# Performance work log

Hardware: AMD Instinct MI355X
Metric: run time of the kernel (lower is better)

## Reference

```python
import jax, jax.numpy as jnp
import numpy as np
from jax import lax

SCALE = 2
NUM_POINTS = 4

def conv2d(x, w, b, pad):
    # x: [B,C,H,W], w: [O,I,kh,kw]
    y = lax.conv_general_dilated(x, w, (1, 1), [(pad, pad), (pad, pad)],
                                 dimension_numbers=("NCHW", "OIHW", "NCHW"))
    return y + b[None, :, None, None]

def grid_sample_border(feat, grid):
    # feat: [B,C,H,W]; grid: [B,Hg,Wg,2] in [-1,1] (x,y), align_corners=False,
    # padding_mode='border' (coordinates clipped before interpolation, as in torch).
    B, C, H, W = feat.shape
    Hg, Wg = grid.shape[1], grid.shape[2]
    gx = jnp.clip((grid[..., 0] + 1.0) * W / 2.0 - 0.5, 0.0, W - 1.0)
    gy = jnp.clip((grid[..., 1] + 1.0) * H / 2.0 - 0.5, 0.0, H - 1.0)
    x0 = jnp.floor(gx); y0 = jnp.floor(gy)
    fx = (gx - x0).reshape(B, 1, -1)
    fy = (gy - y0).reshape(B, 1, -1)
    x0i = jnp.clip(x0.astype(jnp.int32), 0, W - 1)
    y0i = jnp.clip(y0.astype(jnp.int32), 0, H - 1)
    x1i = jnp.clip(x0i + 1, 0, W - 1)
    y1i = jnp.clip(y0i + 1, 0, H - 1)
    featf = feat.reshape(B, C, H * W)
    def gather(yi, xi):
        idx = (yi * W + xi).reshape(B, 1, -1)
        return jnp.take_along_axis(featf, idx, axis=2)  # [B,C,Hg*Wg]
    v00 = gather(y0i, x0i); v01 = gather(y0i, x1i)
    v10 = gather(y1i, x0i); v11 = gather(y1i, x1i)
    out = (v00 * (1 - fx) * (1 - fy) + v01 * fx * (1 - fy)
           + v10 * (1 - fx) * fy + v11 * fx * fy)
    return out.reshape(B, C, Hg, Wg)

def setup_inputs() -> dict:
    key = jax.random.key(0)
    ks = jax.random.split(key, 8)
    B, Cin, Cout, H, W = 8, 256, 256, 64, 64
    high_feat = jax.random.normal(ks[0], (B, Cin, H, W), jnp.float32)
    low_feat = jax.random.normal(ks[1], (B, Cout, H * SCALE, W * SCALE), jnp.float32)
    W1 = jax.random.normal(ks[2], (Cin, Cin + Cout, 1, 1), jnp.float32) * 0.02
    b1 = jnp.zeros((Cin,), jnp.float32)
    # original inits offset_conv2 to zeros; use small random to exercise deformable sampling
    W2 = jax.random.normal(ks[3], (NUM_POINTS * 2, Cin, 3, 3), jnp.float32) * 0.01
    b2 = jnp.zeros((NUM_POINTS * 2,), jnp.float32)
    Wf = jax.random.normal(ks[4], (Cout, Cin, 1, 1), jnp.float32) * 0.05
    bf = jnp.zeros((Cout,), jnp.float32)
    return {"high_feat": high_feat, "low_feat": low_feat, "W1": W1, "b1": b1,
            "W2": W2, "b2": b2, "Wf": Wf, "bf": bf}

def reference(high_feat, low_feat, W1, b1, W2, b2, Wf, bf):
    B, Cin, H, W = high_feat.shape
    H_up, W_up = H * SCALE, W * SCALE
    # bilinear upsample, align_corners=False (half-pixel centers)
    up_high = jax.image.resize(high_feat, (B, Cin, H_up, W_up), method="bilinear")
    concat = jnp.concatenate([up_high, low_feat], axis=1)
    off_feat = jax.nn.relu(conv2d(concat, W1, b1, 0))
    offsets = conv2d(off_feat, W2, b2, 1)  # [B, 2P, H_up, W_up]
    proc = conv2d(high_feat, Wf, bf, 0)    # [B, Cout, H, W]
    # base grid in [-1,1], (x,y)
    gy = jnp.linspace(-1.0, 1.0, H_up)
    gx = jnp.linspace(-1.0, 1.0, W_up)
    base = jnp.stack(jnp.meshgrid(gx, gy, indexing="xy"), axis=-1)  # [H_up,W_up,2]
    # offsets -> [B,P,2,H,W] -> [P,B,H,W,2], normalized to [-1,1] units
    off = offsets.reshape(B, NUM_POINTS, 2, H_up, W_up).transpose(1, 0, 3, 4, 2)
    norm = jnp.array([W_up, H_up], jnp.float32)
    off = off / norm * 2.0
    grids = base[None, None] + off  # [P,B,H_up,W_up,2]
    sampled = jax.vmap(lambda g: grid_sample_border(proc, g))(grids)  # [P,B,C,H_up,W_up]
    return jnp.mean(sampled, axis=0)
```

## Files before the change

### kernel.cpp

```cpp
#include <hip/hip_runtime.h>
#include <stdint.h>

#define NB   8
#define CH   256
#define HW0  4096
#define HW2  16384

typedef __attribute__((ext_vector_type(8))) short short8;
typedef __attribute__((ext_vector_type(8))) unsigned short u16x8;
typedef __attribute__((ext_vector_type(4))) unsigned short u16x4;
typedef __attribute__((ext_vector_type(4))) float floatx4;

__device__ inline unsigned short f2bf(float f) {
    union { float f; uint32_t u; } v; v.f = f;
    return (unsigned short)((v.u + 0x7FFFu + ((v.u >> 16) & 1u)) >> 16);
}
__device__ inline float bf2f(unsigned short h) {
    union { uint32_t u; float f; } v; v.u = ((uint32_t)h) << 16;
    return v.f;
}

__global__ __launch_bounds__(256) void ktrans(const float* __restrict__ src,
        unsigned short* __restrict__ dst, int M) {
    const int b = blockIdx.z, k0 = blockIdx.y * 32, m0 = blockIdx.x * 128;
    const int tid = threadIdx.x;
    __shared__ unsigned short tile[32][132];
    const float* s = src + ((size_t)b * CH + k0) * M + m0;
    for (int c = tid; c < 1024; c += 256) {
        int kk = c >> 5, mm = (c & 31) * 4;
        float4 v = *(const float4*)(s + (size_t)kk * M + mm);
        u16x4 o = { f2bf(v.x), f2bf(v.y), f2bf(v.z), f2bf(v.w) };
        *(u16x4*)&tile[kk][mm] = o;
    }
    __syncthreads();
    unsigned short* d = dst + ((size_t)b * M + m0) * CH + k0;
    for (int c = tid; c < 512; c += 256) {
        int mm = c >> 2, kc = (c & 3) * 8;
        u16x8 v;
        #pragma unroll
        for (int i = 0; i < 8; ++i) v[i] = tile[kc + i][mm];
        *(u16x8*)(d + (size_t)mm * CH + kc) = v;
    }
}

__global__ __launch_bounds__(256) void kwconv(const float* __restrict__ W1,
        const float* __restrict__ Wf, unsigned short* __restrict__ A1,
        unsigned short* __restrict__ A2) {
    int i = blockIdx.x * 256 + threadIdx.x;
    if (i < 512 * 256) {
        int n = i >> 8, k = i & 255;
        float v = (n < 256) ? W1[n * 512 + k] : Wf[(size_t)(n - 256) * 256 + k];
        A1[i] = f2bf(v);
    }
    if (i < 256 * 256) {
        int n = i >> 8, k = i & 255;
        A2[i] = f2bf(W1[n * 512 + 256 + k]);
    }
}

__global__ __launch_bounds__(256) void kwpack(const float* __restrict__ W2v,
        unsigned short* __restrict__ W3p) {
    int i = blockIdx.x * 256 + threadIdx.x;
    if (i >= 9 * 16 * 256) return;
    int ci = i & 255, o = (i >> 8) & 15, t = i >> 12;
    float v = (o < 8) ? W2v[((size_t)o * 256 + ci) * 9 + t] : 0.0f;
    W3p[i] = f2bf(v);
}

__global__ __launch_bounds__(256) void k1_mfma(
    const unsigned short* __restrict__ highT,
    const unsigned short* __restrict__ A1,
    const float* __restrict__ bfv,
    float* __restrict__ T, float* __restrict__ proc)
{
    const int b = blockIdx.z;
    const int m0 = blockIdx.x * 128;
    const int n0 = blockIdx.y * 128;
    const int tid = threadIdx.x;
    __shared__ unsigned short As[128 * 40];
    __shared__ unsigned short Xs[128 * 40];
    const int lane = tid & 63, wid = tid >> 6;
    const int wn = (wid >> 1) * 64, wm = (wid & 1) * 64;
    const int l15 = lane & 15, quad = lane >> 4;

    floatx4 acc[4][4];
    #pragma unroll
    for (int i = 0; i < 4; ++i)
        #pragma unroll
        for (int j = 0; j < 4; ++j)
            acc[i][j] = (floatx4){0.f, 0.f, 0.f, 0.f};

    const unsigned short* Xg = highT + ((size_t)b * HW0 + m0) * CH;

    for (int k0 = 0; k0 < 256; k0 += 32) {
        for (int c = tid; c < 512; c += 256) {
            int row = c >> 2, kc = (c & 3) * 8;
            *(u16x8*)&As[row * 40 + kc] =
                *(const u16x8*)(A1 + (size_t)(n0 + row) * CH + k0 + kc);
            *(u16x8*)&Xs[row * 40 + kc] =
                *(const u16x8*)(Xg + (size_t)row * CH + k0 + kc);
        }
        __syncthreads();
        short8 af[4], bfr[4];
        #pragma unroll
        for (int i = 0; i < 4; ++i)
            af[i] = *(const short8*)&As[(wn + i * 16 + l15) * 40 + quad * 8];
        #pragma unroll
        for (int j = 0; j < 4; ++j)
            bfr[j] = *(const short8*)&Xs[(wm + j * 16 + l15) * 40 + quad * 8];
        #pragma unroll
        for (int i = 0; i < 4; ++i)
            #pragma unroll
            for (int j = 0; j < 4; ++j)
                acc[i][j] = __builtin_amdgcn_mfma_f32_16x16x32_bf16(
                    af[i], bfr[j], acc[i][j], 0, 0, 0);
        __syncthreads();
    }

    const bool isT = (n0 < 256);
    #pragma unroll
    for (int i = 0; i < 4; ++i) {
        int nb = n0 + wn + i * 16 + quad * 4;
        #pragma unroll
        for (int r = 0; r < 4; ++r) {
            int n = nb + r;
            #pragma unroll
            for (int j = 0; j < 4; ++j) {
                int m = m0 + wm + j * 16 + l15;
                float v = acc[i][j][r];
                if (isT) T[((size_t)b * CH + n) * HW0 + m] = v;
                else proc[((size_t)b * CH + n - 256) * HW0 + m] = v + bfv[n - 256];
            }
        }
    }
}

__global__ __launch_bounds__(256) void k2_mfma(
    const unsigned short* __restrict__ lowT,
    const unsigned short* __restrict__ A2,
    const float* __restrict__ b1, const float* __restrict__ T,
    unsigned short* __restrict__ off_featT)
{
    const int b = blockIdx.z;
    const int m0 = blockIdx.x * 128;
    const int n0 = blockIdx.y * 128;
    const int tid = threadIdx.x;
    __shared__ unsigned short smem[2 * 128 * 40];
    unsigned short* As = smem;
    unsigned short* Xs = smem + 128 * 40;
    const int lane = tid & 63, wid = tid >> 6;
    const int wn = (wid >> 1) * 64, wm = (wid & 1) * 64;
    const int l15 = lane & 15, quad = lane >> 4;

    floatx4 acc[4][4];
    #pragma unroll
    for (int i = 0; i < 4; ++i)
        #pragma unroll
        for (int j = 0; j < 4; ++j)
            acc[i][j] = (floatx4){0.f, 0.f, 0.f, 0.f};

    const unsigned short* Xg = lowT + ((size_t)b * HW2 + m0) * CH;

    for (int k0 = 0; k0 < 256; k0 += 32) {
        for (int c = tid; c < 512; c += 256) {
            int row = c >> 2, kc = (c & 3) * 8;
            *(u16x8*)&As[row * 40 + kc] =
                *(const u16x8*)(A2 + (size_t)(n0 + row) * CH + k0 + kc);
            *(u16x8*)&Xs[row * 40 + kc] =
                *(const u16x8*)(Xg + (size_t)row * CH + k0 + kc);
        }
        __syncthreads();
        short8 af[4], bfr[4];
        #pragma unroll
        for (int i = 0; i < 4; ++i)
            af[i] = *(const short8*)&As[(wn + i * 16 + l15) * 40 + quad * 8];
        #pragma unroll
        for (int j = 0; j < 4; ++j)
            bfr[j] = *(const short8*)&Xs[(wm + j * 16 + l15) * 40 + quad * 8];
        #pragma unroll
        for (int i = 0; i < 4; ++i)
            #pragma unroll
            for (int j = 0; j < 4; ++j)
                acc[i][j] = __builtin_amdgcn_mfma_f32_16x16x32_bf16(
                    af[i], bfr[j], acc[i][j], 0, 0, 0);
        __syncthreads();
    }

    const int y = blockIdx.x;
    int hk = y >> 1;
    int yA, yB; float wyA, wyB;
    if (y & 1) { yA = hk; yB = min(hk + 1, 63); wyA = 0.75f; wyB = 0.25f; }
    else       { yB = hk; yA = max(hk - 1, 0);  wyA = 0.25f; wyB = 0.75f; }

    int xA[4], xB[4]; float wxA[4], wxB[4];
    #pragma unroll
    for (int j = 0; j < 4; ++j) {
        int x = wm + j * 16 + l15;
        int xk = x >> 1;
        if (x & 1) { xA[j] = xk; xB[j] = min(xk + 1, 63); wxA[j] = 0.75f; wxB[j] = 0.25f; }
        else       { xB[j] = xk; xA[j] = max(xk - 1, 0);  wxA[j] = 0.25f; wxB[j] = 0.75f; }
    }

    #pragma unroll
    for (int i = 0; i < 4; ++i) {
        int nb = n0 + wn + i * 16 + quad * 4;
        #pragma unroll
        for (int r = 0; r < 4; ++r) {
            int n = nb + r;
            const float* tb  = T + ((size_t)b * CH + n) * HW0;
            const float* trA = tb + yA * 64;
            const float* trB = tb + yB * 64;
            float bias = b1[n];
            #pragma unroll
            for (int j = 0; j < 4; ++j) {
                float up = wyA * (wxA[j] * trA[xA[j]] + wxB[j] * trA[xB[j]])
                         + wyB * (wxA[j] * trB[xA[j]] + wxB[j] * trB[xB[j]]);
                acc[i][j][r] = fmaxf(acc[i][j][r] + up + bias, 0.0f);
            }
        }
    }

    unsigned short (*tile)[136] = (unsigned short (*)[136])smem;
    for (int xh = 0; xh < 2; ++xh) {
        __syncthreads();
        if ((wid & 1) == xh) {
            #pragma unroll
            for (int i = 0; i < 4; ++i) {
                int nc = wn + i * 16 + quad * 4;
                #pragma unroll
                for (int j = 0; j < 4; ++j) {
                    int xr = j * 16 + l15;
                    unsigned int lo = (unsigned int)f2bf(acc[i][j][0])
                                    | ((unsigned int)f2bf(acc[i][j][1]) << 16);
                    unsigned int hi = (unsigned int)f2bf(acc[i][j][2])
                                    | ((unsigned int)f2bf(acc[i][j][3]) << 16);
                    *(unsigned int*)&tile[xr][nc]     = lo;
                    *(unsigned int*)&tile[xr][nc + 2] = hi;
                }
            }
        }
        __syncthreads();
        for (int c = tid; c < 1024; c += 256) {
            int xr = c >> 4, nc = (c & 15) * 8;
            u16x8 v = *(u16x8*)&tile[xr][nc];
            *(u16x8*)(off_featT +
                ((size_t)b * HW2 + (size_t)y * 128 + xh * 64 + xr) * CH + n0 + nc) = v;
        }
    }
}

__global__ __launch_bounds__(256) void k3_mfma(
    const unsigned short* __restrict__ offT,
    const unsigned short* __restrict__ W3p,
    float* __restrict__ offs)
{
    const int b = blockIdx.y;
    const int y = blockIdx.x;
    const int tid = threadIdx.x;
    const int lane = tid & 63, w = tid >> 6;
    const int l15 = lane & 15, quad = lane >> 4;

    floatx4 acc[2];
    acc[0] = (floatx4){0.f, 0.f, 0.f, 0.f};
    acc[1] = (floatx4){0.f, 0.f, 0.f, 0.f};

    const unsigned short* xb = offT + (size_t)b * HW2 * CH;
    const int xbase = w * 32 + l15;

    for (int k0 = 0; k0 < 256; k0 += 32) {
        #pragma unroll
        for (int t = 0; t < 9; ++t) {
            const int dy = t / 3 - 1, dx = t % 3 - 1;
            const int yy = y + dy;
            if ((unsigned)yy >= 128u) continue;
            short8 bw = *(const short8*)(W3p + (size_t)(t * 16 + l15) * CH
                                         + k0 + quad * 8);
            const unsigned short* rowp = xb + ((size_t)yy * 128) * CH + k0 + quad * 8;
            #pragma unroll
            for (int j = 0; j < 2; ++j) {
                int xx = xbase + j * 16 + dx;
                short8 ax = (short8){0, 0, 0, 0, 0, 0, 0, 0};
                if ((unsigned)xx < 128u)
                    ax = *(const short8*)(rowp + (size_t)xx * CH);
                acc[j] = __builtin_amdgcn_mfma_f32_16x16x32_bf16(
                    ax, bw, acc[j], 0, 0, 0);
            }
        }
    }

    if (l15 < 8) {
        float* ob = offs + ((size_t)b * 8 + l15) * HW2 + (size_t)y * 128;
        #pragma unroll
        for (int j = 0; j < 2; ++j) {
            int xpix = w * 32 + j * 16 + quad * 4;
            *(floatx4*)(ob + xpix) = acc[j];
        }
    }
}

__global__ __launch_bounds__(256) void k4_sample(
    const float* __restrict__ offs, const float* __restrict__ b2v,
    const float* __restrict__ proc, float* __restrict__ out)
{
    const int bz = blockIdx.z;
    const int b = bz >> 2, cq = bz & 3;
    const int y = blockIdx.y;
    const int xt = blockIdx.x;
    const int tid = threadIdx.x;

    __shared__ int   sx0[4][64], sy0[4][64];
    __shared__ float sfx[4][64], sfy[4][64];

    if (tid < 64) {
        int x = xt * 64 + tid;
        float gxb = (2.0f * x) / 127.0f - 1.0f;
        float gyb = (2.0f * y) / 127.0f - 1.0f;
        const float* ob = offs + (size_t)b * 8 * HW2 + y * 128 + x;
        #pragma unroll
        for (int p = 0; p < 4; ++p) {
            float ox = ob[(2 * p) * HW2] + b2v[2 * p];
            float oy = ob[(2 * p + 1) * HW2] + b2v[2 * p + 1];
            float gx = gxb + ox * (2.0f / 128.0f);
            float gy = gyb + oy * (2.0f / 128.0f);
            float gxp = fminf(fmaxf((gx + 1.0f) * 32.0f - 0.5f, 0.0f), 63.0f);
            float gyp = fminf(fmaxf((gy + 1.0f) * 32.0f - 0.5f, 0.0f), 63.0f);
            float x0 = floorf(gxp), y0f = floorf(gyp);
            sx0[p][tid] = (int)x0;
            sy0[p][tid] = (int)y0f;
            sfx[p][tid] = gxp - x0;
            sfy[p][tid] = gyp - y0f;
        }
    }
    __syncthreads();

    const int xl = tid & 63;
    const int cl = tid >> 6;
    const int x = xt * 64 + xl;

    int px0[4], py0[4]; float pfx[4], pfy[4];
    #pragma unroll
    for (int p = 0; p < 4; ++p) {
        px0[p] = sx0[p][xl]; py0[p] = sy0[p][xl];
        pfx[p] = sfx[p][xl]; pfy[p] = sfy[p][xl];
    }

    #pragma unroll 4
    for (int i = 0; i < 16; ++i) {
        int c = cq * 64 + i * 4 + cl;
        const float* pb = proc + ((size_t)b * CH + c) * HW0;
        float acc = 0.f;
        #pragma unroll
        for (int p = 0; p < 4; ++p) {
            int x0 = px0[p], y0i = py0[p];
            int x1 = min(x0 + 1, 63), y1 = min(y0i + 1, 63);
            float fx = pfx[p], fy = pfy[p];
            float v00 = pb[y0i * 64 + x0];
            float v01 = pb[y0i * 64 + x1];
            float v10 = pb[y1 * 64 + x0];
            float v11 = pb[y1 * 64 + x1];
            float top = v00 + fx * (v01 - v00);
            float bot = v10 + fx * (v11 - v10);
            acc += top + fy * (bot - top);
        }
        out[(((size_t)b * CH + c) * 128 + y) * 128 + x] = acc * 0.25f;
    }
}

extern "C" void kernel_launch(void* const* d_in, const int* in_sizes, int n_in,
                              void* d_out, int out_size, void* d_ws, size_t ws_size,
                              hipStream_t stream) {
    const float* high = (const float*)d_in[0];
    const float* low  = (const float*)d_in[1];
    const float* W1   = (const float*)d_in[2];
    const float* b1   = (const float*)d_in[3];
    const float* W2v  = (const float*)d_in[4];
    const float* b2v  = (const float*)d_in[5];
    const float* Wf   = (const float*)d_in[6];
    const float* bfv  = (const float*)d_in[7];
    float* out = (float*)d_out;
    float* ws  = (float*)d_ws;

    float* T    = ws;
    float* proc = ws + 8388608;
    float* offs = ws + 16777216;
    unsigned short* highT = (unsigned short*)(ws + 17825792);
    unsigned short* A1 = highT + 8388608;
    unsigned short* A2 = A1 + 131072;

    unsigned short* W3p = highT;

    unsigned short* lowT      = (unsigned short*)out;
    unsigned short* off_featT = ((unsigned short*)out) + 33554432;

    ktrans<<<dim3(32, 8, NB), 256, 0, stream>>>(high, highT, HW0);
    ktrans<<<dim3(128, 8, NB), 256, 0, stream>>>(low, lowT, HW2);
    kwconv<<<dim3(512), 256, 0, stream>>>(W1, Wf, A1, A2);

    k1_mfma<<<dim3(32, 4, NB), 256, 0, stream>>>(highT, A1, bfv, T, proc);
    kwpack<<<dim3(144), 256, 0, stream>>>(W2v, W3p);
    k2_mfma<<<dim3(128, 2, NB), 256, 0, stream>>>(lowT, A2, b1, T, off_featT);
    k3_mfma<<<dim3(128, NB), 256, 0, stream>>>(off_featT, W3p, offs);
    k4_sample<<<dim3(2, 128, NB * 4), 256, 0, stream>>>(offs, b2v, proc, out);
}
```

Measured before the change: 585.9 us.

## Store proc channel-last and gather channel-contiguous in sampling kernel

The proc output of k1 is now written transposed to [B, HW, C] through an LDS staging tile, so every bilinear corner fetch in k4 reads 64 consecutive channels with coalesced loads instead of scattered per-channel gathers. k4 is restructured so each block handles all 256 channels for 64 pixels. Each wave accumulates 16 pixels at a time, then transposes the results through LDS to write NCHW output coalesced. Precomputed corner index and offset packing reduce per-sample address math. The cost is the extra LDS transpose and syncs in k1 and k4, and fewer, larger k4 blocks.

```diff
diff --git a/kernel.cpp b/kernel.cpp
--- a/kernel.cpp
+++ b/kernel.cpp
@@ -71,14 +71,15 @@
     const unsigned short* __restrict__ highT,
     const unsigned short* __restrict__ A1,
     const float* __restrict__ bfv,
-    float* __restrict__ T, float* __restrict__ proc)
+    float* __restrict__ T, float* __restrict__ procT)
 {
     const int b = blockIdx.z;
     const int m0 = blockIdx.x * 128;
     const int n0 = blockIdx.y * 128;
     const int tid = threadIdx.x;
-    __shared__ unsigned short As[128 * 40];
-    __shared__ unsigned short Xs[128 * 40];
+    __shared__ __attribute__((aligned(16))) unsigned short smem[2 * 128 * 40];
+    unsigned short* As = smem;
+    unsigned short* Xs = smem + 128 * 40;
     const int lane = tid & 63, wid = tid >> 6;
     const int wn = (wid >> 1) * 64, wm = (wid & 1) * 64;
     const int l15 = lane & 15, quad = lane >> 4;
@@ -117,19 +118,48 @@
         __syncthreads();
     }
 
-    const bool isT = (n0 < 256);
-    #pragma unroll
-    for (int i = 0; i < 4; ++i) {
-        int nb = n0 + wn + i * 16 + quad * 4;
-        #pragma unroll
-        for (int r = 0; r < 4; ++r) {
-            int n = nb + r;
-            #pragma unroll
-            for (int j = 0; j < 4; ++j) {
-                int m = m0 + wm + j * 16 + l15;
-                float v = acc[i][j][r];
-                if (isT) T[((size_t)b * CH + n) * HW0 + m] = v;
-                else proc[((size_t)b * CH + n - 256) * HW0 + m] = v + bfv[n - 256];
+    if (n0 < 256) {
+        #pragma unroll
+        for (int i = 0; i < 4; ++i) {
+            int nb = n0 + wn + i * 16 + quad * 4;
+            #pragma unroll
+            for (int r = 0; r < 4; ++r) {
+                int n = nb + r;
+                #pragma unroll
+                for (int j = 0; j < 4; ++j) {
+                    int m = m0 + wm + j * 16 + l15;
+                    T[((size_t)b * CH + n) * HW0 + m] = acc[i][j][r];
+                }
+            }
+        }
+    } else {
+        float* tf = (float*)smem;
+        const int nc = n0 - 256;
+        #pragma unroll
+        for (int mq = 0; mq < 4; ++mq) {
+            __syncthreads();
+            if ((wid & 1) == (mq >> 1)) {
+                #pragma unroll
+                for (int jj = 0; jj < 2; ++jj) {
+                    int j = (mq & 1) * 2 + jj;
+                    int ml = j * 16 + l15 - (mq & 1) * 32;
+                    #pragma unroll
+                    for (int i = 0; i < 4; ++i) {
+                        int nl = wn + i * 16 + quad * 4;
+                        #pragma unroll
+                        for (int r = 0; r < 4; ++r)
+                            tf[ml * 132 + nl + r] = acc[i][j][r] + bfv[nc + nl + r];
+                    }
+                }
+            }
+            __syncthreads();
+            int mm = tid >> 3;
+            int c8 = tid & 7;
+            float* dst = procT + ((size_t)b * HW0 + m0 + mq * 32 + mm) * CH + nc;
+            #pragma unroll
+            for (int k = 0; k < 4; ++k) {
+                int col = c8 * 4 + k * 32;
+                *(float4*)(dst + col) = *(const float4*)&tf[mm * 132 + col];
             }
         }
     }
@@ -300,16 +330,18 @@
 
 __global__ __launch_bounds__(256) void k4_sample(
     const float* __restrict__ offs, const float* __restrict__ b2v,
-    const float* __restrict__ proc, float* __restrict__ out)
+    const float* __restrict__ procT, float* __restrict__ out)
 {
-    const int bz = blockIdx.z;
-    const int b = bz >> 2, cq = bz & 3;
-    const int y = blockIdx.y;
-    const int xt = blockIdx.x;
+    const int blk = blockIdx.x;
+    const int b  = blk & 7;
+    const int r  = blk >> 3;
+    const int y  = r >> 1;
+    const int xt = r & 1;
     const int tid = threadIdx.x;
-
-    __shared__ int   sx0[4][64], sy0[4][64];
-    __shared__ float sfx[4][64], sfy[4][64];
+    const int lane = tid & 63, w = tid >> 6;
+
+    __shared__ float4 sp[4][64];
+    __shared__ float tile[4][16 * 65];
 
     if (tid < 64) {
         int x = xt * 64 + tid;
@@ -324,45 +356,53 @@
             float gy = gyb + oy * (2.0f / 128.0f);
             float gxp = fminf(fmaxf((gx + 1.0f) * 32.0f - 0.5f, 0.0f), 63.0f);
             float gyp = fminf(fmaxf((gy + 1.0f) * 32.0f - 0.5f, 0.0f), 63.0f);
-            float x0 = floorf(gxp), y0f = floorf(gyp);
-            sx0[p][tid] = (int)x0;
-            sy0[p][tid] = (int)y0f;
-            sfx[p][tid] = gxp - x0;
-            sfy[p][tid] = gyp - y0f;
+            float x0f = floorf(gxp), y0f = floorf(gyp);
+            int x0 = (int)x0f, y0 = (int)y0f;
+            int idx = (y0 * 64 + x0) * 256;
+            int dxo = (x0 < 63) ? 256 : 0;
+            int dyo = (y0 < 63) ? 16384 : 0;
+            sp[p][tid] = make_float4(__int_as_float(idx),
+                                     __int_as_float(dxo | (dyo << 16)),
+                                     gxp - x0f, gyp - y0f);
         }
     }
     __syncthreads();
 
-    const int xl = tid & 63;
-    const int cl = tid >> 6;
-    const int x = xt * 64 + xl;
-
-    int px0[4], py0[4]; float pfx[4], pfy[4];
-    #pragma unroll
-    for (int p = 0; p < 4; ++p) {
-        px0[p] = sx0[p][xl]; py0[p] = sy0[p][xl];
-        pfx[p] = sfx[p][xl]; pfy[p] = sfy[p][xl];
-    }
-
-    #pragma unroll 4
-    for (int i = 0; i < 16; ++i) {
-        int c = cq * 64 + i * 4 + cl;
-        const float* pb = proc + ((size_t)b * CH + c) * HW0;
-        float acc = 0.f;
-        #pragma unroll
-        for (int p = 0; p < 4; ++p) {
-            int x0 = px0[p], y0i = py0[p];
-            int x1 = min(x0 + 1, 63), y1 = min(y0i + 1, 63);
-            float fx = pfx[p], fy = pfy[p];
-            float v00 = pb[y0i * 64 + x0];
-            float v01 = pb[y0i * 64 + x1];
-            float v10 = pb[y1 * 64 + x0];
-            float v11 = pb[y1 * 64 + x1];
-            float top = v00 + fx * (v01 - v00);
-            float bot = v10 + fx * (v11 - v10);
-            acc += top + fy * (bot - top);
-        }
-        out[(((size_t)b * CH + c) * 128 + y) * 128 + x] = acc * 0.25f;
+    const float* P = procT + (size_t)b * HW0 * CH + w * 64 + lane;
+    float* tw = &tile[w][0];
+    float* outb = out + ((size_t)b * CH + w * 64) * HW2 + (size_t)y * 128 + xt * 64;
+
+    for (int chunk = 0; chunk < 4; ++chunk) {
+        float a[16];
+        #pragma unroll
+        for (int i = 0; i < 16; ++i) a[i] = 0.f;
+        #pragma unroll
+        for (int i = 0; i < 16; ++i) {
+            int px = chunk * 16 + i;
+            #pragma unroll
+            for (int p = 0; p < 4; ++p) {
+                float4 s = sp[p][px];
+                int idx  = __float_as_int(s.x);
+                int pack = __float_as_int(s.y);
+                int dxo = pack & 0xFFFF, dyo = pack >> 16;
+                const float* q = P + idx;
+                float v00 = q[0];
+                float v01 = q[dxo];
+                float v10 = q[dyo];
+                float v11 = q[dyo + dxo];
+                float top = v00 + s.z * (v01 - v00);
+                float bot = v10 + s.z * (v11 - v10);
+                a[i] += top + s.w * (bot - top);
+            }
+        }
+        #pragma unroll
+        for (int i = 0; i < 16; ++i) tw[i * 65 + lane] = a[i] * 0.25f;
+        #pragma unroll
+        for (int g = 0; g < 16; ++g) {
+            int c   = g * 4 + (lane >> 4);
+            int pxl = lane & 15;
+            outb[(size_t)c * HW2 + chunk * 16 + pxl] = tw[pxl * 65 + c];
+        }
     }
 }
 
@@ -380,9 +420,9 @@
     float* out = (float*)d_out;
     float* ws  = (float*)d_ws;
 
-    float* T    = ws;
-    float* proc = ws + 8388608;
-    float* offs = ws + 16777216;
+    float* T     = ws;
+    float* procT = ws + 8388608;
+    float* offs  = ws + 16777216;
     unsigned short* highT = (unsigned short*)(ws + 17825792);
     unsigned short* A1 = highT + 8388608;
     unsigned short* A2 = A1 + 131072;
@@ -396,9 +436,9 @@
     ktrans<<<dim3(128, 8, NB), 256, 0, stream>>>(low, lowT, HW2);
     kwconv<<<dim3(512), 256, 0, stream>>>(W1, Wf, A1, A2);
 
-    k1_mfma<<<dim3(32, 4, NB), 256, 0, stream>>>(highT, A1, bfv, T, proc);
+    k1_mfma<<<dim3(32, 4, NB), 256, 0, stream>>>(highT, A1, bfv, T, procT);
     kwpack<<<dim3(144), 256, 0, stream>>>(W2v, W3p);
     k2_mfma<<<dim3(128, 2, NB), 256, 0, stream>>>(lowT, A2, b1, T, off_featT);
     k3_mfma<<<dim3(128, NB), 256, 0, stream>>>(off_featT, W3p, offs);
-    k4_sample<<<dim3(2, 128, NB * 4), 256, 0, stream>>>(offs, b2v, proc, out);
-}
+    k4_sample<<<dim3(2048), 256, 0, stream>>>(offs, b2v, procT, out);
+}
```

Result: faster. 551.0 us (-6.0%).
